# Kernel optimization log

Hardware: AMD Instinct MI355X
Metric: run time of the kernel (lower is better)

Reference implementation:

```python
import jax, jax.numpy as jnp
import numpy as np

B, C, H, W = 16, 256, 32, 32
N_HEAD, DIM_HEAD = 8, 32  # dim_hidden = 256 == C


def setup_inputs() -> dict:
    key = jax.random.key(0)
    ks = jax.random.split(key, 9)
    s = 1.0 / np.sqrt(C)
    return {
        "x": jax.random.normal(ks[0], (B, C, H, W), dtype=jnp.float32),
        "w_q": jax.random.normal(ks[1], (C, C), dtype=jnp.float32) * s,
        "b_q": jnp.zeros((C,), dtype=jnp.float32),
        "w_k": jax.random.normal(ks[2], (C, C), dtype=jnp.float32) * s,
        "b_k": jnp.zeros((C,), dtype=jnp.float32),
        "w_v": jax.random.normal(ks[3], (C, C), dtype=jnp.float32) * s,
        "b_v": jnp.zeros((C,), dtype=jnp.float32),
        "w_o": jax.random.normal(ks[4], (C, C), dtype=jnp.float32) * s,
        "b_o": jnp.zeros((C,), dtype=jnp.float32),
    }


def reference(x, w_q, b_q, w_k, b_k, w_v, b_v, w_o, b_o):
    b, c, h, w = x.shape
    L = h * w
    scale = DIM_HEAD ** (-0.5)
    xf = x.reshape(b, c, L)  # [b, c, L]

    def proj(wm, bm):
        # 1x1 conv == per-position linear over channels
        y = jnp.einsum('oc,bcl->bol', wm, xf) + bm[None, :, None]
        return y.reshape(b, N_HEAD, DIM_HEAD, L)

    q = proj(w_q, b_q) * scale
    k = proj(w_k, b_k)
    v = proj(w_v, b_v)

    sim = jnp.einsum('bndl,bndm->bnlm', q, k)           # [b, n, L, L]
    att = jax.nn.softmax(sim, axis=-1)
    out = jnp.einsum('bnlm,bndm->bndl', att, v)         # [b, n, d, L]
    out = out.reshape(b, c, L)
    out = jnp.einsum('oc,bcl->bol', w_o, out) + b_o[None, :, None]
    return out.reshape(b, c, h, w)
```

## Files before the change

### kernel.cpp

```cpp
#include <hip/hip_runtime.h>
#include <hip/hip_bf16.h>
#include <math.h>

namespace {
constexpr int B_ = 16, C_ = 256, L_ = 1024, NH_ = 8, DH_ = 32;

typedef __attribute__((ext_vector_type(8))) short short8v;
typedef __attribute__((ext_vector_type(4))) float float4v;

__device__ __forceinline__ short f2bf(float f) {
    unsigned u = __builtin_bit_cast(unsigned, f);
    u += 0x7fffu + ((u >> 16) & 1u);
    return (short)(u >> 16);
}
__device__ __forceinline__ float bf2f(short s) {
    unsigned u = ((unsigned)(unsigned short)s) << 16;
    return __builtin_bit_cast(float, u);
}
__device__ __forceinline__ unsigned pkrn(float a, float b) {
    float2 f; f.x = a; f.y = b;
    __hip_bfloat162 h = __float22bfloat162_rn(f);
    unsigned u;
    __builtin_memcpy(&u, &h, sizeof(u));
    return u;
}
__device__ __forceinline__ void gld16(const short* g, short* l) {
    __builtin_amdgcn_global_load_lds(
        (const __attribute__((address_space(1))) unsigned*)g,
        (__attribute__((address_space(3))) unsigned*)l, 16, 0, 0);
}

__global__ __launch_bounds__(256) void xpose_kernel(
    const float* __restrict__ x, short* __restrict__ xthi)
{
    const int lt = blockIdx.x, ct = blockIdx.y, b = blockIdx.z;
    const int t = threadIdx.x;
    __shared__ float sX[64][68];

#pragma unroll
    for (int e = 0; e < 4; ++e) {
        const int row = e * 16 + (t >> 4);
        const int col = (t & 15) * 4;
        float4 v = *(const float4*)&x[((size_t)b * C_ + ct * 64 + row) * L_ + lt * 64 + col];
        *(float4*)&sX[row][col] = v;
    }
    __syncthreads();

    const int l = t & 63, cg = t >> 6;
    short hi[16];
#pragma unroll
    for (int i = 0; i < 16; ++i) hi[i] = f2bf(sX[cg * 16 + i][l]);
    const size_t base = ((size_t)b * L_ + lt * 64 + l) * C_ + ct * 64 + cg * 16;
    *(short8v*)&xthi[base]     = *(short8v*)&hi[0];
    *(short8v*)&xthi[base + 8] = *(short8v*)&hi[8];
}

__global__ __launch_bounds__(256) void stackw_kernel(
    const float* __restrict__ wq, const float* __restrict__ wk,
    const float* __restrict__ wv, const float* __restrict__ wo,
    short* __restrict__ WA, short* __restrict__ WoA)
{
    const int g = blockIdx.x * 256 + threadIdx.x;
    if (g < 768 * 256) {
        const int o = g >> 8, cc = g & 255;
        const float* src = (o < 256) ? wq : (o < 512) ? wk : wv;
        const float v = src[(size_t)(o & 255) * 256 + cc];
        const short hi = f2bf(v);
        const short lo = f2bf(v - bf2f(hi));
        WA[(size_t)o * 512 + cc]       = hi;
        WA[(size_t)o * 512 + 256 + cc] = lo;
    } else {
        const int g2 = g - 768 * 256;
        const int o = g2 >> 8, cc = g2 & 255;
        const float v = wo[(size_t)o * 256 + cc];
        const short hi = f2bf(v);
        const short lo = f2bf(v - bf2f(hi));
        WoA[(size_t)o * 512 + cc]       = hi;
        WoA[(size_t)o * 512 + 256 + cc] = lo;
    }
}

template <int KTOT, int EPI>
__global__ __launch_bounds__(256, 3) void gemm_kernel(
    const short* __restrict__ A, const short* __restrict__ B0,
    const float* __restrict__ bias0, const float* __restrict__ bias1, const float* __restrict__ bias2,
    float qscale, void* __restrict__ out0, void* __restrict__ out1, void* __restrict__ out2)
{
    const int lt = blockIdx.x, ot = blockIdx.y, b = blockIdx.z;
    const int t = threadIdx.x, wv = t >> 6, lane = t & 63;
    const int quad = lane >> 4, c = lane & 15;
    const int wo = (wv & 1) * 64, wl = (wv >> 1) * 64;

    __shared__ short sA[128 * 64];
    __shared__ short sB[128 * 64];

    float4v acc[4][4];
#pragma unroll
    for (int i = 0; i < 4; ++i)
#pragma unroll
        for (int j = 0; j < 4; ++j) acc[i][j] = (float4v)0.f;

    const short* Arow = A + (size_t)(ot * 128) * KTOT;
    const int srow = t >> 3, sseg = t & 7;
    const int seg = sseg ^ (srow & 7);

    for (int kk = 0; kk < KTOT / 64; ++kk) {
        __syncthreads();
#pragma unroll
        for (int e = 0; e < 4; ++e) {
            gld16(Arow + (size_t)(e * 32 + srow) * KTOT + kk * 64 + seg * 8,
                  &sA[(e * 256 + t) * 8]);
            gld16(B0 + ((size_t)b * L_ + lt * 128 + e * 32 + srow) * 256 + (kk & 3) * 64 + seg * 8,
                  &sB[(e * 256 + t) * 8]);
        }
        __syncthreads();

#pragma unroll
        for (int kc2 = 0; kc2 < 2; ++kc2) {
            short8v af[4], bf[4];
#pragma unroll
            for (int i = 0; i < 4; ++i) {
                const int row = wo + 16 * i + c;
                af[i] = *(const short8v*)&sA[row * 64 + (((kc2 * 4 + quad) ^ (c & 7)) * 8)];
            }
#pragma unroll
            for (int j = 0; j < 4; ++j) {
                const int row = wl + 16 * j + c;
                bf[j] = *(const short8v*)&sB[row * 64 + (((kc2 * 4 + quad) ^ (c & 7)) * 8)];
            }
#pragma unroll
            for (int i = 0; i < 4; ++i)
#pragma unroll
                for (int j = 0; j < 4; ++j)
                    acc[i][j] = __builtin_amdgcn_mfma_f32_16x16x32_bf16(af[i], bf[j], acc[i][j], 0, 0, 0);
        }
    }

    if constexpr (EPI == 0) {
        const int typ = ot >> 1;
        const int chbase = (ot & 1) * 128 + wo;
        const float* bp = (typ == 0) ? bias0 : (typ == 1) ? bias1 : bias2;
        const float sc = (typ == 0) ? qscale : 1.f;
        short* outp = (short*)((typ == 0) ? out0 : (typ == 1) ? out1 : out2);
        if (typ < 2) {
#pragma unroll
            for (int i = 0; i < 4; ++i) {
                const int ch0 = chbase + 16 * i + quad * 4;
                const int head = ch0 >> 5, d0 = ch0 & 31;
                float bias[4];
#pragma unroll
                for (int r = 0; r < 4; ++r) bias[r] = bp[ch0 + r];
#pragma unroll
                for (int j = 0; j < 4; ++j) {
                    const int l = lt * 128 + wl + 16 * j + c;
                    short4 sv;
                    sv.x = f2bf((acc[i][j][0] + bias[0]) * sc);
                    sv.y = f2bf((acc[i][j][1] + bias[1]) * sc);
                    sv.z = f2bf((acc[i][j][2] + bias[2]) * sc);
                    sv.w = f2bf((acc[i][j][3] + bias[3]) * sc);
                    *(short4*)&outp[(((size_t)b * NH_ + head) * L_ + l) * 32 + d0] = sv;
                }
            }
        } else {
#pragma unroll
            for (int i = 0; i < 4; ++i)
#pragma unroll
                for (int r = 0; r < 4; ++r) {
                    const int ch = chbase + 16 * i + quad * 4 + r;
                    const float bias = bp[ch];
#pragma unroll
                    for (int j = 0; j < 4; ++j)
                        outp[((size_t)b * C_ + ch) * L_ + lt * 128 + wl + 16 * j + c] =
                            f2bf(acc[i][j][r] + bias);
                }
        }
    } else {
        float* outp = (float*)out0;
#pragma unroll
        for (int i = 0; i < 4; ++i)
#pragma unroll
            for (int r = 0; r < 4; ++r) {
                const int ch = ot * 128 + wo + 16 * i + quad * 4 + r;
                const float bias = bias0[ch];
#pragma unroll
                for (int j = 0; j < 4; ++j)
                    outp[((size_t)b * C_ + ch) * L_ + lt * 128 + wl + 16 * j + c] =
                        acc[i][j][r] + bias;
            }
    }
}

__global__ __launch_bounds__(256, 4) void attn_kernel(
    const short* __restrict__ qt,
    const short* __restrict__ kt,
    const short* __restrict__ vb,
    short* __restrict__ athi)
{
    const int flat = blockIdx.x;
    const int g = ((flat >> 6) << 3) | (flat & 7);
    const int chunk = (flat >> 3) & 7;
    const int b = g >> 3, h = g & 7;
    const int t = threadIdx.x;
    const int wv = t >> 6, lane = t & 63;
    const int quad = lane >> 4, c = lane & 15;
    const int lq0 = chunk * 128 + wv * 32;

    __shared__ __align__(16) short sK[64 * 32];
    __shared__ __align__(16) short sV[2][32 * 32];
    __shared__ __align__(16) short sPT[2][4][2][16][64];

    const size_t bh = (size_t)b * NH_ + h;
    const short* qbase = qt + (bh * L_) * 32;
    const short* kbase = kt + (bh * L_) * 32;
    const size_t vrow = (size_t)b * C_ + h * DH_;

    short8v qfrag[2];
#pragma unroll
    for (int qf = 0; qf < 2; ++qf)
        qfrag[qf] = *(const short8v*)(qbase + (size_t)(lq0 + qf * 16 + c) * 32 + quad * 8);

    float lp4[2][4];
#pragma unroll
    for (int qf = 0; qf < 2; ++qf)
#pragma unroll
        for (int r = 0; r < 4; ++r) lp4[qf][r] = 0.f;
    float4v o_acc[2][2];
#pragma unroll
    for (int qf = 0; qf < 2; ++qf) { o_acc[qf][0] = (float4v)0.f; o_acc[qf][1] = (float4v)0.f; }

    auto stage = [&](int m0) {
        gld16(kbase + (size_t)(m0 + (t >> 2)) * 32 + (t & 3) * 8, &sK[t * 8]);
        gld16(vb + (vrow + ((t >> 2) & 31)) * L_ + m0 + (t >> 7) * 32 + (t & 3) * 8,
              (short*)sV + t * 8);
    };

    stage(0);

    short8v vfp[2][2];

    for (int i = 0; i <= 16; ++i) {
        short8v kf[4], vf[2][2];
        if (i < 16) {
            __syncthreads();
#pragma unroll
            for (int kb = 0; kb < 4; ++kb)
                kf[kb] = *(const short8v*)&sK[(kb * 16 + c) * 32 + quad * 8];
#pragma unroll
            for (int kc = 0; kc < 2; ++kc)
#pragma unroll
                for (int nb2 = 0; nb2 < 2; ++nb2)
                    vf[kc][nb2] = *(const short8v*)&sV[kc][(nb2 * 16 + c) * 32 + quad * 8];
            __syncthreads();
            if (i < 15) stage((i + 1) * 64);
        }

        if (i > 0) {
            const int pb = (i - 1) & 1;
#pragma unroll
            for (int qf = 0; qf < 2; ++qf)
#pragma unroll
                for (int kc = 0; kc < 2; ++kc) {
                    const int G = (kc * 4 + quad) ^ (c & 7);
                    const short8v pf = *(const short8v*)&sPT[pb][wv][qf][c][G * 8];
#pragma unroll
                    for (int nb2 = 0; nb2 < 2; ++nb2)
                        o_acc[qf][nb2] = __builtin_amdgcn_mfma_f32_16x16x32_bf16(vfp[kc][nb2], pf, o_acc[qf][nb2], 0, 0, 0);
                }
        }

        if (i < 16) {
            const int cb = i & 1;
            float4v st[2][4];
#pragma unroll
            for (int qf = 0; qf < 2; ++qf)
#pragma unroll
                for (int kb = 0; kb < 4; ++kb)
                    st[qf][kb] = __builtin_amdgcn_mfma_f32_16x16x32_bf16(kf[kb], qfrag[qf], (float4v)0.f, 0, 0, 0);
#pragma unroll
            for (int qf = 0; qf < 2; ++qf)
#pragma unroll
                for (int kb = 0; kb < 4; ++kb) {
                    float p[4];
#pragma unroll
                    for (int r = 0; r < 4; ++r) {
                        p[r] = __builtin_amdgcn_exp2f(st[qf][kb][r]);
                        lp4[qf][r] += p[r];
                    }
                    uint2 w;
                    w.x = pkrn(p[0], p[1]);
                    w.y = pkrn(p[2], p[3]);
                    const int Gw = (kb * 2 + (quad >> 1)) ^ (c & 7);
                    *(uint2*)&sPT[cb][wv][qf][c][Gw * 8 + (quad & 1) * 4] = w;
                }
#pragma unroll
            for (int kc = 0; kc < 2; ++kc)
#pragma unroll
                for (int nb2 = 0; nb2 < 2; ++nb2) vfp[kc][nb2] = vf[kc][nb2];
        }
    }

#pragma unroll
    for (int qf = 0; qf < 2; ++qf) {
        float l = (lp4[qf][0] + lp4[qf][1]) + (lp4[qf][2] + lp4[qf][3]);
        l += __shfl_xor(l, 16);
        l += __shfl_xor(l, 32);
        const float inv = 1.f / l;
#pragma unroll
        for (int nb2 = 0; nb2 < 2; ++nb2) {
            short4 sv;
            sv.x = f2bf(o_acc[qf][nb2][0] * inv);
            sv.y = f2bf(o_acc[qf][nb2][1] * inv);
            sv.z = f2bf(o_acc[qf][nb2][2] * inv);
            sv.w = f2bf(o_acc[qf][nb2][3] * inv);
            *(short4*)&athi[((size_t)b * L_ + lq0 + qf * 16 + c) * C_ + h * DH_ + nb2 * 16 + quad * 4] = sv;
        }
    }
}

}

extern "C" void kernel_launch(void* const* d_in, const int* in_sizes, int n_in,
                              void* d_out, int out_size, void* d_ws, size_t ws_size,
                              hipStream_t stream) {
    const float* x   = (const float*)d_in[0];
    const float* w_q = (const float*)d_in[1];
    const float* b_q = (const float*)d_in[2];
    const float* w_k = (const float*)d_in[3];
    const float* b_k = (const float*)d_in[4];
    const float* w_v = (const float*)d_in[5];
    const float* b_v = (const float*)d_in[6];
    const float* w_o = (const float*)d_in[7];
    const float* b_o = (const float*)d_in[8];
    float* out = (float*)d_out;

    const size_t NT = (size_t)B_ * L_ * C_;
    short* xthi = (short*)d_ws;
    short* WA   = xthi + NT;
    short* WoA  = WA + 768 * 512;
    short* qt   = WoA + 256 * 512;
    short* kt   = qt + NT;
    short* vb   = kt + NT;
    short* athi = vb + NT;

    const float scale_q = 0.17677669529663687f * 1.4426950408889634f;

    xpose_kernel<<<dim3(L_ / 64, C_ / 64, B_), 256, 0, stream>>>(x, xthi);
    stackw_kernel<<<dim3(1024), 256, 0, stream>>>(w_q, w_k, w_v, w_o, WA, WoA);
    gemm_kernel<512, 0><<<dim3(L_ / 128, 6, B_), 256, 0, stream>>>(
        WA, xthi, b_q, b_k, b_v, scale_q, qt, kt, vb);
    attn_kernel<<<dim3(1024), 256, 0, stream>>>(qt, kt, vb, athi);
    gemm_kernel<512, 1><<<dim3(L_ / 128, 2, B_), 256, 0, stream>>>(
        WoA, athi, b_o, nullptr, nullptr, 1.f, out, nullptr, nullptr);
}
```

Measured before the change: 150.7 us.

## Double-buffer K/V in attention, swizzle LDS staging, merge prep kernels

The attention kernel now double-buffers the K/V tiles. It issues the next tile's async global-to-LDS load right after a single barrier per iteration, instead of loading between two barriers. The K/V staging layout is XOR-swizzled so the fragment reads spread across LDS banks, and the probability tile is reduced to one buffer per wave. The transpose/convert kernel and the weight-splitting kernel are fused into one launch to save a launch. The cost is more LDS for K/V, and correctness now depends on each wave reading its own P tile in order between iterations.

```diff
diff --git a/kernel.cpp b/kernel.cpp
--- a/kernel.cpp
+++ b/kernel.cpp
@@ -30,53 +30,53 @@
         (__attribute__((address_space(3))) unsigned*)l, 16, 0, 0);
 }
 
-__global__ __launch_bounds__(256) void xpose_kernel(
-    const float* __restrict__ x, short* __restrict__ xthi)
-{
-    const int lt = blockIdx.x, ct = blockIdx.y, b = blockIdx.z;
-    const int t = threadIdx.x;
-    __shared__ float sX[64][68];
-
-#pragma unroll
-    for (int e = 0; e < 4; ++e) {
-        const int row = e * 16 + (t >> 4);
-        const int col = (t & 15) * 4;
-        float4 v = *(const float4*)&x[((size_t)b * C_ + ct * 64 + row) * L_ + lt * 64 + col];
-        *(float4*)&sX[row][col] = v;
-    }
-    __syncthreads();
-
-    const int l = t & 63, cg = t >> 6;
-    short hi[16];
-#pragma unroll
-    for (int i = 0; i < 16; ++i) hi[i] = f2bf(sX[cg * 16 + i][l]);
-    const size_t base = ((size_t)b * L_ + lt * 64 + l) * C_ + ct * 64 + cg * 16;
-    *(short8v*)&xthi[base]     = *(short8v*)&hi[0];
-    *(short8v*)&xthi[base + 8] = *(short8v*)&hi[8];
-}
-
-__global__ __launch_bounds__(256) void stackw_kernel(
+__global__ __launch_bounds__(256) void prep_kernel(
+    const float* __restrict__ x, short* __restrict__ xthi,
     const float* __restrict__ wq, const float* __restrict__ wk,
     const float* __restrict__ wv, const float* __restrict__ wo,
     short* __restrict__ WA, short* __restrict__ WoA)
 {
-    const int g = blockIdx.x * 256 + threadIdx.x;
-    if (g < 768 * 256) {
-        const int o = g >> 8, cc = g & 255;
-        const float* src = (o < 256) ? wq : (o < 512) ? wk : wv;
-        const float v = src[(size_t)(o & 255) * 256 + cc];
-        const short hi = f2bf(v);
-        const short lo = f2bf(v - bf2f(hi));
-        WA[(size_t)o * 512 + cc]       = hi;
-        WA[(size_t)o * 512 + 256 + cc] = lo;
+    const int bid = blockIdx.x;
+    const int t = threadIdx.x;
+    __shared__ float sX[64][68];
+
+    if (bid < 1024) {
+        const int lt = bid & 15, ct = (bid >> 4) & 3, b = bid >> 6;
+#pragma unroll
+        for (int e = 0; e < 4; ++e) {
+            const int row = e * 16 + (t >> 4);
+            const int col = (t & 15) * 4;
+            float4 v = *(const float4*)&x[((size_t)b * C_ + ct * 64 + row) * L_ + lt * 64 + col];
+            *(float4*)&sX[row][col] = v;
+        }
+        __syncthreads();
+
+        const int l = t & 63, cg = t >> 6;
+        short hi[16];
+#pragma unroll
+        for (int i = 0; i < 16; ++i) hi[i] = f2bf(sX[cg * 16 + i][l]);
+        const size_t base = ((size_t)b * L_ + lt * 64 + l) * C_ + ct * 64 + cg * 16;
+        *(short8v*)&xthi[base]     = *(short8v*)&hi[0];
+        *(short8v*)&xthi[base + 8] = *(short8v*)&hi[8];
     } else {
-        const int g2 = g - 768 * 256;
-        const int o = g2 >> 8, cc = g2 & 255;
-        const float v = wo[(size_t)o * 256 + cc];
-        const short hi = f2bf(v);
-        const short lo = f2bf(v - bf2f(hi));
-        WoA[(size_t)o * 512 + cc]       = hi;
-        WoA[(size_t)o * 512 + 256 + cc] = lo;
+        const int g = (bid - 1024) * 256 + t;
+        if (g < 768 * 256) {
+            const int o = g >> 8, cc = g & 255;
+            const float* src = (o < 256) ? wq : (o < 512) ? wk : wv;
+            const float v = src[(size_t)(o & 255) * 256 + cc];
+            const short hi = f2bf(v);
+            const short lo = f2bf(v - bf2f(hi));
+            WA[(size_t)o * 512 + cc]       = hi;
+            WA[(size_t)o * 512 + 256 + cc] = lo;
+        } else {
+            const int g2 = g - 768 * 256;
+            const int o = g2 >> 8, cc = g2 & 255;
+            const float v = wo[(size_t)o * 256 + cc];
+            const short hi = f2bf(v);
+            const short lo = f2bf(v - bf2f(hi));
+            WoA[(size_t)o * 512 + cc]       = hi;
+            WoA[(size_t)o * 512 + 256 + cc] = lo;
+        }
     }
 }
 
@@ -205,9 +205,9 @@
     const int quad = lane >> 4, c = lane & 15;
     const int lq0 = chunk * 128 + wv * 32;
 
-    __shared__ __align__(16) short sK[64 * 32];
-    __shared__ __align__(16) short sV[2][32 * 32];
-    __shared__ __align__(16) short sPT[2][4][2][16][64];
+    __shared__ __align__(16) short sK[2][64 * 32];
+    __shared__ __align__(16) short sV[2][2][32 * 32];
+    __shared__ __align__(16) short sPT[4][2][16][64];
 
     const size_t bh = (size_t)b * NH_ + h;
     const short* qbase = qt + (bh * L_) * 32;
@@ -228,13 +228,16 @@
 #pragma unroll
     for (int qf = 0; qf < 2; ++qf) { o_acc[qf][0] = (float4v)0.f; o_acc[qf][1] = (float4v)0.f; }
 
-    auto stage = [&](int m0) {
-        gld16(kbase + (size_t)(m0 + (t >> 2)) * 32 + (t & 3) * 8, &sK[t * 8]);
-        gld16(vb + (vrow + ((t >> 2) & 31)) * L_ + m0 + (t >> 7) * 32 + (t & 3) * 8,
-              (short*)sV + t * 8);
+    const int sseg = (t & 3) ^ ((t >> 3) & 3);
+    const int rsw = (c >> 1) & 3;
+
+    auto stage = [&](int m0, int buf) {
+        gld16(kbase + (size_t)(m0 + (t >> 2)) * 32 + sseg * 8, &sK[buf][t * 8]);
+        gld16(vb + (vrow + ((t >> 2) & 31)) * L_ + m0 + (t >> 7) * 32 + sseg * 8,
+              (short*)sV[buf] + t * 8);
     };
 
-    stage(0);
+    stage(0, 0);
 
     short8v vfp[2][2];
 
@@ -242,26 +245,26 @@
         short8v kf[4], vf[2][2];
         if (i < 16) {
             __syncthreads();
+            if (i < 15) stage((i + 1) * 64, (i + 1) & 1);
+            const short* Kb = sK[i & 1];
+            const short* Vb = (const short*)sV[i & 1];
 #pragma unroll
             for (int kb = 0; kb < 4; ++kb)
-                kf[kb] = *(const short8v*)&sK[(kb * 16 + c) * 32 + quad * 8];
+                kf[kb] = *(const short8v*)&Kb[(kb * 16 + c) * 32 + ((quad ^ rsw) * 8)];
 #pragma unroll
             for (int kc = 0; kc < 2; ++kc)
 #pragma unroll
                 for (int nb2 = 0; nb2 < 2; ++nb2)
-                    vf[kc][nb2] = *(const short8v*)&sV[kc][(nb2 * 16 + c) * 32 + quad * 8];
-            __syncthreads();
-            if (i < 15) stage((i + 1) * 64);
+                    vf[kc][nb2] = *(const short8v*)&Vb[kc * 1024 + (nb2 * 16 + c) * 32 + ((quad ^ rsw) * 8)];
         }
 
         if (i > 0) {
-            const int pb = (i - 1) & 1;
 #pragma unroll
             for (int qf = 0; qf < 2; ++qf)
 #pragma unroll
                 for (int kc = 0; kc < 2; ++kc) {
                     const int G = (kc * 4 + quad) ^ (c & 7);
-                    const short8v pf = *(const short8v*)&sPT[pb][wv][qf][c][G * 8];
+                    const short8v pf = *(const short8v*)&sPT[wv][qf][c][G * 8];
 #pragma unroll
                     for (int nb2 = 0; nb2 < 2; ++nb2)
                         o_acc[qf][nb2] = __builtin_amdgcn_mfma_f32_16x16x32_bf16(vfp[kc][nb2], pf, o_acc[qf][nb2], 0, 0, 0);
@@ -269,7 +272,6 @@
         }
 
         if (i < 16) {
-            const int cb = i & 1;
             float4v st[2][4];
 #pragma unroll
             for (int qf = 0; qf < 2; ++qf)
@@ -290,7 +292,7 @@
                     w.x = pkrn(p[0], p[1]);
                     w.y = pkrn(p[2], p[3]);
                     const int Gw = (kb * 2 + (quad >> 1)) ^ (c & 7);
-                    *(uint2*)&sPT[cb][wv][qf][c][Gw * 8 + (quad & 1) * 4] = w;
+                    *(uint2*)&sPT[wv][qf][c][Gw * 8 + (quad & 1) * 4] = w;
                 }
 #pragma unroll
             for (int kc = 0; kc < 2; ++kc)
@@ -344,8 +346,7 @@
 
     const float scale_q = 0.17677669529663687f * 1.4426950408889634f;
 
-    xpose_kernel<<<dim3(L_ / 64, C_ / 64, B_), 256, 0, stream>>>(x, xthi);
-    stackw_kernel<<<dim3(1024), 256, 0, stream>>>(w_q, w_k, w_v, w_o, WA, WoA);
+    prep_kernel<<<dim3(2048), 256, 0, stream>>>(x, xthi, w_q, w_k, w_v, w_o, WA, WoA);
     gemm_kernel<512, 0><<<dim3(L_ / 128, 6, B_), 256, 0, stream>>>(
         WA, xthi, b_q, b_k, b_v, scale_q, qt, kt, vb);
     attn_kernel<<<dim3(1024), 256, 0, stream>>>(qt, kt, vb, athi);
```

After: 144.6 us. 1.04x faster.
